# Kernel optimization log

Hardware: AMD Instinct MI355X
Metric: run time of the kernel (lower is better)

Reference implementation:

```python
import jax, jax.numpy as jnp
import numpy as np

T, B, E, H = 2048, 2, 1024, 16
Dh = E // H


def setup_inputs() -> dict:
    key = jax.random.key(0)
    ks = jax.random.split(key, 5)
    s = 0.02
    query = jax.random.normal(ks[0], (T, B, E), dtype=jnp.float32)
    Wq = jax.random.normal(ks[1], (E, E), dtype=jnp.float32) * s
    Wk = jax.random.normal(ks[2], (E, E), dtype=jnp.float32) * s
    Wv = jax.random.normal(ks[3], (E, E), dtype=jnp.float32) * s
    Wo = jax.random.normal(ks[4], (E, E), dtype=jnp.float32) * s
    bq = jnp.zeros((E,), jnp.float32)
    bk = jnp.zeros((E,), jnp.float32)
    bv = jnp.zeros((E,), jnp.float32)
    bo = jnp.zeros((E,), jnp.float32)
    # additive causal mask: 0 on/below diagonal, -inf above (standard fairseq usage)
    neg = jnp.finfo(jnp.float32).min
    attn_mask = jnp.where(jnp.triu(jnp.ones((T, T), jnp.bool_), k=1), neg, 0.0).astype(jnp.float32)
    return {"query": query, "Wq": Wq, "bq": bq, "Wk": Wk, "bk": bk,
            "Wv": Wv, "bv": bv, "Wo": Wo, "bo": bo, "attn_mask": attn_mask}


def reference(query, Wq, bq, Wk, bk, Wv, bv, Wo, bo, attn_mask):
    t, b, e = query.shape
    scale = Dh ** -0.5
    # self-attention projections (nn.Linear: x @ W.T + b)
    q = (query @ Wq.T + bq) * scale  # [T,B,E]
    k = query @ Wk.T + bk
    v = query @ Wv.T + bv
    # [T, B*H, Dh] -> [B*H, T, Dh]
    q = q.reshape(t, b * H, Dh).transpose(1, 0, 2)
    k = k.reshape(t, b * H, Dh).transpose(1, 0, 2)
    v = v.reshape(t, b * H, Dh).transpose(1, 0, 2)
    # explicit bmm -> softmax -> bmm (materializes [B*H, T, T])
    attn_weights = jnp.einsum('btd,bsd->bts', q, k) + attn_mask[None, :, :]
    attn_probs = jax.nn.softmax(attn_weights, axis=-1)
    attn = jnp.einsum('bts,bsd->btd', attn_probs, v)  # [B*H, T, Dh]
    attn = attn.transpose(1, 0, 2).reshape(t, b, e)  # [T,B,E]
    out = attn @ Wo.T + bo
    return out
```

## Files before the change

### kernel.cpp

```cpp
#include <hip/hip_runtime.h>


typedef __attribute__((ext_vector_type(8))) short   s16x8;
typedef __attribute__((ext_vector_type(4))) float   f32x4;
typedef __attribute__((ext_vector_type(2))) __fp16  f16x2;
typedef __attribute__((ext_vector_type(4))) __fp16  f16x4;

#define MFMA16(a, b, c) __builtin_amdgcn_mfma_f32_16x16x32_bf16((a), (b), (c), 0, 0, 0)
#define MFMApv(a, b, c) __builtin_amdgcn_mfma_f32_16x16x16f16((a), (b), (c), 0, 0, 0)

static __device__ __forceinline__ unsigned short f2bf(float f) {
    unsigned u = __float_as_uint(f);
    unsigned r = u + 0x7fffu + ((u >> 16) & 1u);
    return (unsigned short)(r >> 16);
}

static __device__ __forceinline__ void gl2lds16(const void* g, void* l) {
    __builtin_amdgcn_global_load_lds(
        (const __attribute__((address_space(1))) unsigned int*)g,
        (__attribute__((address_space(3))) unsigned int*)l, 16, 0, 0);
}

__global__ __launch_bounds__(256) void cvt_all(const float* __restrict__ query,
                                               const float* __restrict__ w0,
                                               const float* __restrict__ w1,
                                               const float* __restrict__ w2,
                                               const float* __restrict__ w3,
                                               unsigned short* __restrict__ Xb,
                                               unsigned short* __restrict__ Wcat) {
    const int bx = blockIdx.x;
    if (bx < 4096) {
        const int i = threadIdx.x;
        const float4 f = reinterpret_cast<const float4*>(query + (size_t)bx * 1024)[i];
        ushort4 u;
        u.x = f2bf(f.x); u.y = f2bf(f.y); u.z = f2bf(f.z); u.w = f2bf(f.w);
        const int mrow = (bx & 1) * 2048 + (bx >> 1);
        reinterpret_cast<ushort4*>(Xb + (size_t)mrow * 1024)[i] = u;
    } else {
        const int j   = bx - 4096;
        const int sel = j >> 10;
        const int i   = (j & 1023) * 256 + threadIdx.x;
        const float* src = (sel == 0) ? w0 : (sel == 1) ? w1 : (sel == 2) ? w2 : w3;
        const float4 f = reinterpret_cast<const float4*>(src)[i];
        ushort4 u;
        u.x = f2bf(f.x); u.y = f2bf(f.y); u.z = f2bf(f.z); u.w = f2bf(f.w);
        reinterpret_cast<ushort4*>(Wcat + (size_t)sel * 1048576)[i] = u;
    }
}

__global__ __launch_bounds__(256) void gemm128(const unsigned short* __restrict__ A,
                                               const unsigned short* __restrict__ W,
                                               const float* __restrict__ b0,
                                               const float* __restrict__ b1,
                                               const float* __restrict__ b2,
                                               unsigned short* __restrict__ outQK,
                                               __fp16* __restrict__ outV,
                                               float* __restrict__ outF,
                                               int qkv) {
    __shared__ unsigned short Al[128 * 32];
    __shared__ unsigned short Bl[128 * 32];

    const int tid  = threadIdx.x;
    const int w    = tid >> 6;
    const int lane = tid & 63;
    const int quad = lane >> 4;
    const int c    = lane & 15;
    const int wm   = w >> 1;
    const int wn   = w & 1;

    const int m0 = blockIdx.y * 128;
    const int n0 = blockIdx.x * 128;

    f32x4 acc[4][4];
    #pragma unroll
    for (int mi = 0; mi < 4; ++mi)
        #pragma unroll
        for (int ni = 0; ni < 4; ++ni) acc[mi][ni] = (f32x4){0.f, 0.f, 0.f, 0.f};

    const int srow = tid >> 2;
    const int sci  = (tid & 3) ^ ((tid >> 3) & 3);
    const unsigned short* aG = A + (size_t)(m0 + srow) * 1024 + sci * 8;
    const unsigned short* wG = W + (size_t)(n0 + srow) * 1024 + sci * 8;
    unsigned short* aL = &Al[srow * 32 + (tid & 3) * 8];
    unsigned short* wL = &Bl[srow * 32 + (tid & 3) * 8];

    const int swz = (quad ^ ((c >> 1) & 3)) * 8;

    for (int kk = 0; kk < 32; ++kk) {
        const int k0 = kk * 32;
        __syncthreads();
        gl2lds16(aG + k0,              aL);
        gl2lds16(aG + k0 + 64 * 1024,  aL + 64 * 32);
        gl2lds16(wG + k0,              wL);
        gl2lds16(wG + k0 + 64 * 1024,  wL + 64 * 32);
        __syncthreads();

        s16x8 af[4], bf[4];
        #pragma unroll
        for (int mi = 0; mi < 4; ++mi)
            af[mi] = *reinterpret_cast<const s16x8*>(&Al[(wm * 64 + mi * 16 + c) * 32 + swz]);
        #pragma unroll
        for (int ni = 0; ni < 4; ++ni)
            bf[ni] = *reinterpret_cast<const s16x8*>(&Bl[(wn * 64 + ni * 16 + c) * 32 + swz]);
        #pragma unroll
        for (int mi = 0; mi < 4; ++mi)
            #pragma unroll
            for (int ni = 0; ni < 4; ++ni)
                acc[mi][ni] = MFMA16(af[mi], bf[ni], acc[mi][ni]);
    }

    if (qkv) {
        const int sel = n0 >> 10;
        if (sel < 2) {
            const float scale = (sel == 0) ? 0.18033688011112042f : 1.0f;
            const float* bias = (sel == 0) ? b0 : b1;
            #pragma unroll
            for (int ni = 0; ni < 4; ++ni) {
                const int n = n0 + wn * 64 + ni * 16 + c;
                const float bval = bias[n & 1023];
                #pragma unroll
                for (int mi = 0; mi < 4; ++mi)
                    #pragma unroll
                    for (int r = 0; r < 4; ++r) {
                        const int m = m0 + wm * 64 + mi * 16 + quad * 4 + r;
                        outQK[(size_t)m * 2048 + n] = f2bf((acc[mi][ni][r] + bval) * scale);
                    }
            }
        } else {
            #pragma unroll
            for (int ni = 0; ni < 4; ++ni) {
                const int vcol = n0 - 2048 + wn * 64 + ni * 16 + c;
                const int h = vcol >> 6, d = vcol & 63;
                const float bval = b2[vcol];
                #pragma unroll
                for (int mi = 0; mi < 4; ++mi) {
                    const int m = m0 + wm * 64 + mi * 16 + quad * 4;
                    const int bb = m >> 11, t = m & 2047;
                    const f16x2 lo = __builtin_amdgcn_cvt_pkrtz(acc[mi][ni][0] + bval,
                                                                acc[mi][ni][1] + bval);
                    const f16x2 hi = __builtin_amdgcn_cvt_pkrtz(acc[mi][ni][2] + bval,
                                                                acc[mi][ni][3] + bval);
                    uint2 st;
                    st.x = __builtin_bit_cast(unsigned int, lo);
                    st.y = __builtin_bit_cast(unsigned int, hi);
                    *reinterpret_cast<uint2*>(outV + ((size_t)((bb * 16 + h) * 64 + d)) * 2048 + t) = st;
                }
            }
        }
    } else {
        #pragma unroll
        for (int ni = 0; ni < 4; ++ni) {
            const int n = n0 + wn * 64 + ni * 16 + c;
            const float bval = b0[n];
            #pragma unroll
            for (int mi = 0; mi < 4; ++mi) {
                const int m = m0 + wm * 64 + mi * 16 + quad * 4;
                const int bb = m >> 11, t = m & 2047;
                #pragma unroll
                for (int r = 0; r < 4; ++r)
                    outF[(size_t)(2 * (t + r) + bb) * 1024 + n] = acc[mi][ni][r] + bval;
            }
        }
    }
}

__global__ __launch_bounds__(256, 2) void attn_kernel(const unsigned short* __restrict__ QKb,
                                                      const __fp16* __restrict__ Vt,
                                                      unsigned short* __restrict__ Ob) {
    __shared__ unsigned short Kl[2][2][64][32];
    __shared__ __fp16 Vl[2][64][64];

    const int tid  = threadIdx.x;
    const int w    = tid >> 6;
    const int lane = tid & 63;
    const int quad = lane >> 4;
    const int c    = lane & 15;

    const int bh = blockIdx.x, bB = bh >> 4, h = bh & 15;
    const int p  = blockIdx.y;
    const int aT[2]   = { 31 - p, p };
    const int trgT[2] = { aT[0] * 64 + w * 16, aT[1] * 64 + w * 16 };
    const int nIt = 32 - p;

    s16x8 aq[2][2];
    #pragma unroll
    for (int t = 0; t < 2; ++t) {
        const unsigned short* qp = QKb + (size_t)(bB * 2048 + trgT[t] + c) * 2048 + h * 64 + quad * 8;
        aq[t][0] = *reinterpret_cast<const s16x8*>(qp);
        aq[t][1] = *reinterpret_cast<const s16x8*>(qp + 32);
    }

    const int lr4 = lane >> 2, sl4 = lane & 3;
    const unsigned short* kSrc = QKb + (size_t)(bB * 2048 + w * 16 + lr4) * 2048
                                 + 1024 + h * 64 + (sl4 ^ ((lane >> 3) & 3)) * 8;
    const int vr8 = lane >> 3, sl8 = lane & 7;
    const __fp16* vSrcA = Vt + (size_t)(bh * 64 + w * 16 + vr8) * 2048 + (sl8 ^ vr8) * 8;
    const __fp16* vSrcB = vSrcA + (size_t)8 * 2048;

    f32x4 acc[2][4];
    float l[2] = {0.f, 0.f};
    #pragma unroll
    for (int t = 0; t < 2; ++t)
        #pragma unroll
        for (int dt = 0; dt < 4; ++dt) acc[t][dt] = (f32x4){0.f, 0.f, 0.f, 0.f};

    const int kswz = (quad ^ ((c >> 1) & 3)) * 8;

    {
        gl2lds16(kSrc,      &Kl[0][0][w * 16 + lr4][sl4 * 8]);
        gl2lds16(kSrc + 32, &Kl[0][1][w * 16 + lr4][sl4 * 8]);
        gl2lds16(vSrcA,     &Vl[0][w * 16 + vr8][sl8 * 8]);
        gl2lds16(vSrcB,     &Vl[0][w * 16 + 8 + vr8][sl8 * 8]);
    }

    for (int it = 0; it < nIt; ++it) {
        const int buf = it & 1;
        __syncthreads();
        if (it + 1 < nIt) {
            const size_t s1 = (size_t)(it + 1) * 64;
            const int nb = buf ^ 1;
            gl2lds16(kSrc + s1 * 2048,      &Kl[nb][0][w * 16 + lr4][sl4 * 8]);
            gl2lds16(kSrc + s1 * 2048 + 32, &Kl[nb][1][w * 16 + lr4][sl4 * 8]);
            gl2lds16(vSrcA + s1,            &Vl[nb][w * 16 + vr8][sl8 * 8]);
            gl2lds16(vSrcB + s1,            &Vl[nb][w * 16 + 8 + vr8][sl8 * 8]);
        }

        s16x8 kf[4][2];
        #pragma unroll
        for (int ns = 0; ns < 4; ++ns) {
            kf[ns][0] = *reinterpret_cast<const s16x8*>(&Kl[buf][0][ns * 16 + c][kswz]);
            kf[ns][1] = *reinterpret_cast<const s16x8*>(&Kl[buf][1][ns * 16 + c][kswz]);
        }
        f16x4 vf[4][4];
        #pragma unroll
        for (int dt = 0; dt < 4; ++dt)
            #pragma unroll
            for (int ch = 0; ch < 4; ++ch) {
                const int phys = ((2 * ch + (quad >> 1)) ^ (c & 7)) * 8 + (quad & 1) * 4;
                vf[dt][ch] = *reinterpret_cast<const f16x4*>(&Vl[buf][dt * 16 + c][phys]);
            }

        const int s0 = it * 64;
        #pragma unroll
        for (int t = 0; t < 2; ++t) {
            if (it > aT[t]) continue;
            const bool diag = (it == aT[t]);
            f32x4 sT[4];
            #pragma unroll
            for (int ns = 0; ns < 4; ++ns) {
                f32x4 z = (f32x4){0.f, 0.f, 0.f, 0.f};
                z = MFMA16(kf[ns][0], aq[t][0], z);
                sT[ns] = MFMA16(kf[ns][1], aq[t][1], z);
            }
            f16x4 pf[4];
            float lp = 0.f;
            #pragma unroll
            for (int ns = 0; ns < 4; ++ns) {
                float pv[4];
                #pragma unroll
                for (int r = 0; r < 4; ++r) pv[r] = exp2f(sT[ns][r]);
                if (diag) {
                    const int sb = s0 + ns * 16 + quad * 4;
                    const int qg = trgT[t] + c;
                    #pragma unroll
                    for (int r = 0; r < 4; ++r) if (sb + r > qg) pv[r] = 0.f;
                }
                lp += (pv[0] + pv[1]) + (pv[2] + pv[3]);
                const f16x2 lo = __builtin_amdgcn_cvt_pkrtz(pv[0], pv[1]);
                const f16x2 hi = __builtin_amdgcn_cvt_pkrtz(pv[2], pv[3]);
                pf[ns] = __builtin_shufflevector(lo, hi, 0, 1, 2, 3);
            }
            l[t] += lp;
            #pragma unroll
            for (int dt = 0; dt < 4; ++dt)
                #pragma unroll
                for (int ns = 0; ns < 4; ++ns)
                    acc[t][dt] = MFMApv(vf[dt][ns], pf[ns], acc[t][dt]);
        }
    }

    #pragma unroll
    for (int t = 0; t < 2; ++t) {
        float lv = l[t];
        lv += __shfl_xor(lv, 16);
        lv += __shfl_xor(lv, 32);
        const float inv = 1.0f / lv;
        const size_t base = (size_t)(bB * 2048 + trgT[t] + c) * 1024 + h * 64;
        #pragma unroll
        for (int dt = 0; dt < 4; ++dt) {
            const unsigned u0 = (unsigned)f2bf(acc[t][dt][0] * inv)
                              | ((unsigned)f2bf(acc[t][dt][1] * inv) << 16);
            const unsigned u1 = (unsigned)f2bf(acc[t][dt][2] * inv)
                              | ((unsigned)f2bf(acc[t][dt][3] * inv) << 16);
            uint2 st; st.x = u0; st.y = u1;
            *reinterpret_cast<uint2*>(Ob + base + dt * 16 + quad * 4) = st;
        }
    }
}

extern "C" void kernel_launch(void* const* d_in, const int* in_sizes, int n_in,
                              void* d_out, int out_size, void* d_ws, size_t ws_size,
                              hipStream_t stream) {
    const float* query = (const float*)d_in[0];
    const float* Wq    = (const float*)d_in[1];
    const float* bq    = (const float*)d_in[2];
    const float* Wk    = (const float*)d_in[3];
    const float* bk    = (const float*)d_in[4];
    const float* Wv    = (const float*)d_in[5];
    const float* bv    = (const float*)d_in[6];
    const float* Wo    = (const float*)d_in[7];
    const float* bo    = (const float*)d_in[8];

    float* out = (float*)d_out;

    unsigned short* ws    = (unsigned short*)d_ws;
    unsigned short* Xbf   = ws;
    unsigned short* Wcat  = Xbf  + (size_t)4096 * 1024;
    unsigned short* QKb   = Wcat + (size_t)4 * 1024 * 1024;
    __fp16*         Vtw   = (__fp16*)(QKb + (size_t)4096 * 2048);
    unsigned short* attnb = (unsigned short*)(Vtw + (size_t)32 * 64 * 2048);

    cvt_all<<<8192, 256, 0, stream>>>(query, Wq, Wk, Wv, Wo, Xbf, Wcat);

    gemm128<<<dim3(24, 32), 256, 0, stream>>>(Xbf, Wcat, bq, bk, bv,
                                              QKb, Vtw, nullptr, 1);

    attn_kernel<<<dim3(32, 16), 256, 0, stream>>>(QKb, Vtw, attnb);

    gemm128<<<dim3(8, 32), 256, 0, stream>>>(attnb, Wcat + (size_t)3 * 1024 * 1024,
                                             bo, nullptr, nullptr, nullptr, nullptr, out, 0);
}
```

Baseline: 217.5 us.

## Double-buffer GEMM LDS tiles and stage V-transpose epilogue through LDS

Splits the GEMM's shared-memory tiles into two buffers. The next K-slice's global-to-LDS loads are issued while MFMAs run on the current slice, which cuts the barriers per iteration from two to one. The V-projection epilogue now writes its fp16 results into a swizzled LDS tile and then stores them to the transposed V layout as contiguous 16-byte chunks, replacing the scattered 8-byte stores. This doubles LDS use per block, which may lower occupancy, and adds an extra barrier plus an LDS round trip in the epilogue.

```diff
diff --git a/kernel.cpp b/kernel.cpp
--- a/kernel.cpp
+++ b/kernel.cpp
@@ -57,8 +57,7 @@
                                                __fp16* __restrict__ outV,
                                                float* __restrict__ outF,
                                                int qkv) {
-    __shared__ unsigned short Al[128 * 32];
-    __shared__ unsigned short Bl[128 * 32];
+    __shared__ __align__(16) unsigned short smem[2][2][128 * 32];
 
     const int tid  = threadIdx.x;
     const int w    = tid >> 6;
@@ -81,27 +80,34 @@
     const int sci  = (tid & 3) ^ ((tid >> 3) & 3);
     const unsigned short* aG = A + (size_t)(m0 + srow) * 1024 + sci * 8;
     const unsigned short* wG = W + (size_t)(n0 + srow) * 1024 + sci * 8;
-    unsigned short* aL = &Al[srow * 32 + (tid & 3) * 8];
-    unsigned short* wL = &Bl[srow * 32 + (tid & 3) * 8];
+    const int soff = srow * 32 + (tid & 3) * 8;
 
     const int swz = (quad ^ ((c >> 1) & 3)) * 8;
 
+    gl2lds16(aG,             &smem[0][0][soff]);
+    gl2lds16(aG + 64 * 1024, &smem[0][0][soff + 64 * 32]);
+    gl2lds16(wG,             &smem[0][1][soff]);
+    gl2lds16(wG + 64 * 1024, &smem[0][1][soff + 64 * 32]);
+
     for (int kk = 0; kk < 32; ++kk) {
-        const int k0 = kk * 32;
+        const int buf = kk & 1;
         __syncthreads();
-        gl2lds16(aG + k0,              aL);
-        gl2lds16(aG + k0 + 64 * 1024,  aL + 64 * 32);
-        gl2lds16(wG + k0,              wL);
-        gl2lds16(wG + k0 + 64 * 1024,  wL + 64 * 32);
-        __syncthreads();
+        if (kk + 1 < 32) {
+            const int k1 = (kk + 1) * 32;
+            const int nb = buf ^ 1;
+            gl2lds16(aG + k1,             &smem[nb][0][soff]);
+            gl2lds16(aG + k1 + 64 * 1024, &smem[nb][0][soff + 64 * 32]);
+            gl2lds16(wG + k1,             &smem[nb][1][soff]);
+            gl2lds16(wG + k1 + 64 * 1024, &smem[nb][1][soff + 64 * 32]);
+        }
 
         s16x8 af[4], bf[4];
         #pragma unroll
         for (int mi = 0; mi < 4; ++mi)
-            af[mi] = *reinterpret_cast<const s16x8*>(&Al[(wm * 64 + mi * 16 + c) * 32 + swz]);
+            af[mi] = *reinterpret_cast<const s16x8*>(&smem[buf][0][(wm * 64 + mi * 16 + c) * 32 + swz]);
         #pragma unroll
         for (int ni = 0; ni < 4; ++ni)
-            bf[ni] = *reinterpret_cast<const s16x8*>(&Bl[(wn * 64 + ni * 16 + c) * 32 + swz]);
+            bf[ni] = *reinterpret_cast<const s16x8*>(&smem[buf][1][(wn * 64 + ni * 16 + c) * 32 + swz]);
         #pragma unroll
         for (int mi = 0; mi < 4; ++mi)
             #pragma unroll
@@ -127,15 +133,15 @@
                     }
             }
         } else {
+            __syncthreads();
+            unsigned short* tile = &smem[0][0][0];
             #pragma unroll
             for (int ni = 0; ni < 4; ++ni) {
-                const int vcol = n0 - 2048 + wn * 64 + ni * 16 + c;
-                const int h = vcol >> 6, d = vcol & 63;
-                const float bval = b2[vcol];
+                const int n = wn * 64 + ni * 16 + c;
+                const float bval = b2[(n0 - 2048) + n];
                 #pragma unroll
                 for (int mi = 0; mi < 4; ++mi) {
-                    const int m = m0 + wm * 64 + mi * 16 + quad * 4;
-                    const int bb = m >> 11, t = m & 2047;
+                    const int m = wm * 64 + mi * 16 + quad * 4;
                     const f16x2 lo = __builtin_amdgcn_cvt_pkrtz(acc[mi][ni][0] + bval,
                                                                 acc[mi][ni][1] + bval);
                     const f16x2 hi = __builtin_amdgcn_cvt_pkrtz(acc[mi][ni][2] + bval,
@@ -143,8 +149,21 @@
                     uint2 st;
                     st.x = __builtin_bit_cast(unsigned int, lo);
                     st.y = __builtin_bit_cast(unsigned int, hi);
-                    *reinterpret_cast<uint2*>(outV + ((size_t)((bb * 16 + h) * 64 + d)) * 2048 + t) = st;
+                    const int phys = n * 128 + (((m >> 3) ^ (n & 15)) << 3) + (m & 7);
+                    *reinterpret_cast<uint2*>(&tile[phys]) = st;
                 }
+            }
+            __syncthreads();
+            const int n = tid >> 1;
+            const int vcol = (n0 - 2048) + n;
+            const int bb = m0 >> 11, tbase = m0 & 2047;
+            __fp16* vdst = outV + ((size_t)((bb * 16 + (vcol >> 6)) * 64 + (vcol & 63))) * 2048 + tbase;
+            #pragma unroll
+            for (int j = 0; j < 8; ++j) {
+                const int lc = (tid & 1) * 8 + j;
+                const int phys = n * 128 + ((lc ^ (n & 15)) << 3);
+                *reinterpret_cast<uint4*>(vdst + lc * 8) =
+                    *reinterpret_cast<const uint4*>(&tile[phys]);
             }
         }
     } else {
```

Measured after the change: 211.0 us. 1.03x faster.
